# Kernel tuning notes

Measured on AMD Instinct MI355X. Metric: run time of the kernel, lower is better.

Reference implementation:

```python
import jax, jax.numpy as jnp
import numpy as np

N_USERS = 50000
N_ITEMS = 50000
E = 400000
S = 128   # in_feats_s (memory / GRU hidden)
T = 64    # in_feats_t (time encoding dim)
ED = 64   # edge feature dim
M = 2 * S + T + ED  # in_feats_m = 384

_BASIS_FREQ = jnp.asarray(1.0 / 10 ** np.linspace(0, 9, T), dtype=jnp.float32)


def time_encode(ts):
    # cos(ts * freq + phase), phase == 0
    return jnp.cos(ts[:, None] * _BASIS_FREQ[None, :])


def mean_message(src_mem, dst_mem, ts, e, src, dst, n_dst):
    # mail per edge: [E, 2S + T + ED]
    mail = jnp.concatenate(
        [src_mem[src], dst_mem[dst], time_encode(ts), e], axis=1)
    s = jax.ops.segment_sum(mail, dst, num_segments=n_dst)
    cnt = jax.ops.segment_sum(jnp.ones_like(ts), dst, num_segments=n_dst)
    return s / jnp.maximum(cnt, 1.0)[:, None]


def gru_step(x, h, w_ih, w_hh, b_ih, b_hh):
    # single-step PyTorch GRU; gate order r, z, n
    gi = x @ w_ih.T + b_ih
    gh = h @ w_hh.T + b_hh
    ir, iz, i_n = jnp.split(gi, 3, axis=1)
    hr, hz, h_n = jnp.split(gh, 3, axis=1)
    r = jax.nn.sigmoid(ir + hr)
    z = jax.nn.sigmoid(iz + hz)
    n = jnp.tanh(i_n + r * h_n)
    return (1.0 - z) * n + z * h


def setup_inputs() -> dict:
    key = jax.random.key(0)
    ks = jax.random.split(key, 16)
    sc = 1.0 / np.sqrt(S)
    return {
        "si":   jax.random.normal(ks[0], (N_USERS, S), jnp.float32),
        "sj":   jax.random.normal(ks[1], (N_ITEMS, S), jnp.float32),
        "si_r": jax.random.normal(ks[2], (N_ITEMS, S), jnp.float32),
        "sj_r": jax.random.normal(ks[3], (N_USERS, S), jnp.float32),
        "t":    jax.random.uniform(ks[4], (E,), jnp.float32),
        "t_r":  jax.random.uniform(ks[5], (E,), jnp.float32),
        "e":    jax.random.normal(ks[6], (E, ED), jnp.float32),
        "e_r":  jax.random.normal(ks[7], (E, ED), jnp.float32),
        "w_ih": jax.random.normal(ks[8], (3 * S, M), jnp.float32) * sc,
        "w_hh": jax.random.normal(ks[9], (3 * S, S), jnp.float32) * sc,
        "b_ih": jax.random.normal(ks[10], (3 * S,), jnp.float32) * sc,
        "b_hh": jax.random.normal(ks[11], (3 * S,), jnp.float32) * sc,
        "src_g":  jax.random.randint(ks[12], (E,), 0, N_USERS, jnp.int32),
        "dst_g":  jax.random.randint(ks[13], (E,), 0, N_ITEMS, jnp.int32),
        "src_gr": jax.random.randint(ks[14], (E,), 0, N_ITEMS, jnp.int32),
        "dst_gr": jax.random.randint(ks[15], (E,), 0, N_USERS, jnp.int32),
    }


def reference(si, sj, si_r, sj_r, t, t_r, e, e_r,
              w_ih, w_hh, b_ih, b_hh,
              src_g, dst_g, src_gr, dst_gr):
    # g: user -> item; g_r: item -> user
    mj = mean_message(si, sj, t, e, src_g, dst_g, N_ITEMS)       # messages to items
    mi = mean_message(si_r, sj_r, t_r, e_r, src_gr, dst_gr, N_USERS)  # messages to users
    si_out = gru_step(mi, sj_r, w_ih, w_hh, b_ih, b_hh)  # user memory update
    sj_out = gru_step(mj, sj, w_ih, w_hh, b_ih, b_hh)    # item memory update
    return (si_out, sj_out)
```

## Files before the change

### kernel.cpp

```cpp
#include <hip/hip_runtime.h>
#include <math.h>

#define NUSERS 50000
#define NITEMS 50000
#define NTOT   100000
#define NNODE  50000
#define NCHUNK 196
#define MTILES 6250
#define KDIM   512

typedef __attribute__((ext_vector_type(4))) float f32x4;
typedef __attribute__((ext_vector_type(8))) short short8;
typedef unsigned int u32;

#define AS1 __attribute__((address_space(1)))
#define AS3 __attribute__((address_space(3)))

static __device__ __forceinline__ unsigned short f2bf(float f) {
  unsigned int u = __float_as_uint(f);
  u += 0x7fffu + ((u >> 16) & 1u);
  return (unsigned short)(u >> 16);
}

static __device__ __forceinline__ void gload_lds16(const void* g, void* l) {
  __builtin_amdgcn_global_load_lds((const AS1 u32*)g, (AS3 u32*)l, 16, 0, 0);
}

__global__ void pack_w_kernel(const float* __restrict__ w_ih,
                              const float* __restrict__ w_hh,
                              const float* __restrict__ b_ih,
                              const float* __restrict__ b_hh,
                              unsigned short* __restrict__ Wb,
                              float* __restrict__ bb) {
  int idx = blockIdx.x * 256 + threadIdx.x;
  int j = idx & 7, l = (idx >> 3) & 63, ktt = idx >> 9;
  int kt = ktt & 15, tt = ktt >> 4;
  int g = tt * 16 + (l & 15);
  int k = kt * 32 + (l >> 4) * 8 + j;
  float v;
  if (g < 256)      v = (k < 384) ? w_ih[g * 384 + k] : w_hh[g * 128 + (k - 384)];
  else if (g < 384) v = (k < 384) ? w_ih[g * 384 + k] : 0.0f;
  else              v = (k < 384) ? 0.0f : w_hh[(g - 128) * 128 + (k - 384)];
  Wb[idx] = f2bf(v);
  if (idx < 512) {
    float b = (idx < 256) ? (b_ih[idx] + b_hh[idx])
            : (idx < 384) ? b_ih[idx]
                          : b_hh[idx - 128];
    bb[idx] = b;
  }
}

__global__ void hist_kernel(const int* __restrict__ dst_g,
                            const int* __restrict__ dst_gr,
                            int* __restrict__ deg_j, int* __restrict__ deg_i, int E) {
  int i = blockIdx.x * 256 + threadIdx.x;
  if (i < E) atomicAdd(&deg_j[dst_g[i]], 1);
  else if (i < 2 * E) atomicAdd(&deg_i[dst_gr[i - E]], 1);
}

__global__ void chunksum_kernel(const int* __restrict__ deg_j,
                                const int* __restrict__ deg_i,
                                int* __restrict__ csum) {
  int c = blockIdx.x;
  const int* deg = (c < NCHUNK) ? deg_j : deg_i;
  int cc = (c < NCHUNK) ? c : c - NCHUNK;
  int t = threadIdx.x;
  int idx = cc * 256 + t;
  int v = (idx < NNODE) ? deg[idx] : 0;
  for (int off = 32; off; off >>= 1) v += __shfl_down(v, off, 64);
  __shared__ int wsum[4];
  if ((t & 63) == 0) wsum[t >> 6] = v;
  __syncthreads();
  if (t == 0) csum[c] = wsum[0] + wsum[1] + wsum[2] + wsum[3];
}

__global__ void chunkscan_kernel(const int* __restrict__ csum, int* __restrict__ coff) {
  int d = blockIdx.x;
  const int* cs = csum + d * NCHUNK;
  int* co = coff + d * NCHUNK;
  int t = threadIdx.x, lane = t & 63, w = t >> 6;
  int v = (t < NCHUNK) ? cs[t] : 0;
  int x = v;
  for (int off = 1; off < 64; off <<= 1) {
    int y = __shfl_up(x, off, 64);
    if (lane >= off) x += y;
  }
  __shared__ int wt[4];
  if (lane == 63) wt[w] = x;
  __syncthreads();
  int add = 0;
  for (int k = 0; k < 4; ++k) if (k < w) add += wt[k];
  if (t < NCHUNK) co[t] = add + x - v;
}

__global__ void localscan_kernel(const int* __restrict__ deg_j,
                                 const int* __restrict__ deg_i,
                                 const int* __restrict__ coff,
                                 int* __restrict__ rs_j, int* __restrict__ cur_j,
                                 int* __restrict__ rs_i, int* __restrict__ cur_i) {
  int c = blockIdx.x;
  bool dj = c < NCHUNK;
  const int* deg = dj ? deg_j : deg_i;
  int cc = dj ? c : c - NCHUNK;
  int* rs = dj ? rs_j : rs_i;
  int* cur = dj ? cur_j : cur_i;
  int base = coff[c];
  int t = threadIdx.x, lane = t & 63, w = t >> 6;
  int idx = cc * 256 + t;
  int v = (idx < NNODE) ? deg[idx] : 0;
  int x = v;
  for (int off = 1; off < 64; off <<= 1) {
    int y = __shfl_up(x, off, 64);
    if (lane >= off) x += y;
  }
  __shared__ int wt[4];
  if (lane == 63) wt[w] = x;
  __syncthreads();
  int add = 0;
  for (int k = 0; k < 4; ++k) if (k < w) add += wt[k];
  int ex = base + add + x - v;
  if (idx < NNODE) { rs[idx] = ex; cur[idx] = ex; }
}

__global__ void fill_kernel(const int* __restrict__ src_g, const int* __restrict__ dst_g,
                            const float* __restrict__ t,
                            const int* __restrict__ src_gr, const int* __restrict__ dst_gr,
                            const float* __restrict__ t_r,
                            int* __restrict__ cur_j, int* __restrict__ cur_i,
                            int4* __restrict__ recP_j, int4* __restrict__ recP_i,
                            int E) {
  int i = blockIdx.x * 256 + threadIdx.x;
  if (i < E) {
    int pos = atomicAdd(&cur_j[dst_g[i]], 1);
    recP_j[pos] = make_int4(src_g[i], i, __float_as_int(t[i]), 0);
  } else if (i < 2 * E) {
    int k = i - E;
    int pos = atomicAdd(&cur_i[dst_gr[k]], 1);
    recP_i[pos] = make_int4(src_gr[k], k, __float_as_int(t_r[k]), 0);
  }
}

__global__ __launch_bounds__(256) void gather_kernel(
    const float* __restrict__ si, const float* __restrict__ sj,
    const float* __restrict__ si_r, const float* __restrict__ sj_r,
    const float* __restrict__ e, const float* __restrict__ e_r,
    const int* __restrict__ rs_j, const int* __restrict__ rs_i,
    const int* __restrict__ deg_j, const int* __restrict__ deg_i,
    const int4* __restrict__ recP_j, const int4* __restrict__ recP_i,
    unsigned short* __restrict__ Xb) {
  __shared__ __align__(16) unsigned short rowbuf[4][512];
  int wid = threadIdx.x >> 6, lane = threadIdx.x & 63;
  int node = blockIdx.x * 4 + wid;
  bool user = node < NUSERS;
  int idx = user ? node : node - NUSERS;
  const float* smem = user ? si_r : si;
  const float* h    = user ? sj_r : sj;
  const float* ef   = user ? e_r : e;
  int start = __builtin_amdgcn_readfirstlane((user ? rs_i : rs_j)[idx]);
  int deg   = __builtin_amdgcn_readfirstlane((user ? deg_i : deg_j)[idx]);
  const int4* rec = user ? recP_i : recP_j;

  float freq = __expf((float)lane * -0.3289407276f);
  float a0 = 0.f, a1 = 0.f, a2 = 0.f, a3 = 0.f;

  for (int i = 0; i < deg; i += 4) {
    int i1 = (i + 1 < deg) ? i + 1 : deg - 1;
    int i2 = (i + 2 < deg) ? i + 2 : deg - 1;
    int i3 = (i + 3 < deg) ? i + 3 : deg - 1;
    int4 r0 = rec[start + i];
    int4 r1 = rec[start + i1];
    int4 r2 = rec[start + i2];
    int4 r3 = rec[start + i3];
    float w1 = (i + 1 < deg) ? 1.0f : 0.0f;
    float w2 = (i + 2 < deg) ? 1.0f : 0.0f;
    float w3 = (i + 3 < deg) ? 1.0f : 0.0f;

    float x00 = smem[(size_t)r0.x * 128 + lane];
    float x01 = smem[(size_t)r0.x * 128 + 64 + lane];
    float f0  = ef[(size_t)r0.y * 64 + lane];
    float x10 = smem[(size_t)r1.x * 128 + lane];
    float x11 = smem[(size_t)r1.x * 128 + 64 + lane];
    float f1  = ef[(size_t)r1.y * 64 + lane];
    float x20 = smem[(size_t)r2.x * 128 + lane];
    float x21 = smem[(size_t)r2.x * 128 + 64 + lane];
    float f2  = ef[(size_t)r2.y * 64 + lane];
    float x30 = smem[(size_t)r3.x * 128 + lane];
    float x31 = smem[(size_t)r3.x * 128 + 64 + lane];
    float f3  = ef[(size_t)r3.y * 64 + lane];

    float c0 = __cosf(__int_as_float(r0.z) * freq);
    float c1 = __cosf(__int_as_float(r1.z) * freq);
    float c2 = __cosf(__int_as_float(r2.z) * freq);
    float c3 = __cosf(__int_as_float(r3.z) * freq);

    a0 += x00 + w1 * x10 + w2 * x20 + w3 * x30;
    a1 += x01 + w1 * x11 + w2 * x21 + w3 * x31;
    a2 += c0  + w1 * c1  + w2 * c2  + w3 * c3;
    a3 += f0  + w1 * f1  + w2 * f2  + w3 * f3;
  }

  float invc = (deg > 0) ? 1.0f / (float)deg : 0.0f;
  float hz   = (deg > 0) ? 1.0f : 0.0f;
  float h0 = h[(size_t)idx * 128 + lane];
  float h1 = h[(size_t)idx * 128 + 64 + lane];

  unsigned short* rb = rowbuf[wid];
  rb[lane]        = f2bf(a0 * invc);
  rb[64  + lane]  = f2bf(a1 * invc);
  rb[128 + lane]  = f2bf(h0 * hz);
  rb[192 + lane]  = f2bf(h1 * hz);
  rb[256 + lane]  = f2bf(a2 * invc);
  rb[320 + lane]  = f2bf(a3 * invc);
  rb[384 + lane]  = f2bf(h0);
  rb[448 + lane]  = f2bf(h1);
  __syncthreads();

  int rt = node >> 4, m = node & 15;
  int kt = lane >> 2, q = lane & 3;
  short8 vv = *(const short8*)(rb + lane * 8);
  *(short8*)(Xb + (((size_t)rt * 16 + kt) * 64 + q * 16 + m) * 8) = vv;
}

__global__ __launch_bounds__(512, 2) void gemm_gru_kernel(
    const unsigned short* __restrict__ Xb,
    const unsigned short* __restrict__ Wb,
    const float* __restrict__ bb,
    const float* __restrict__ sj_r,
    const float* __restrict__ sj,
    float* __restrict__ out) {
  __shared__ __align__(16) unsigned short sB[32768];
  int wid = threadIdx.x >> 6, lane = threadIdx.x & 63;
  int mtile = blockIdx.x * 8 + wid;
  bool valid = mtile < MTILES;
  int col16 = lane & 15, quad = lane >> 4;

  f32x4 acc[32];
#pragma unroll
  for (int t = 0; t < 32; ++t) acc[t] = (f32x4)0.0f;

  const unsigned short* Abase = Xb + (size_t)(valid ? mtile : 0) * 8192;

  for (int s = 0; s < 8; ++s) {
#pragma unroll
    for (int i = 0; i < 8; ++i) {
      int c = wid * 8 + i;
      int tt = c >> 1, kt = s * 2 + (c & 1);
      const unsigned short* g = Wb + ((size_t)(tt * 16 + kt) * 64 + lane) * 8;
      gload_lds16(g, sB + c * 512);
    }
    __syncthreads();
    if (valid) {
      short8 a0 = *(const short8*)(Abase + (size_t)(s * 2) * 512 + lane * 8);
      short8 a1 = *(const short8*)(Abase + (size_t)(s * 2 + 1) * 512 + lane * 8);
#pragma unroll
      for (int t = 0; t < 32; ++t) {
        short8 b0 = *(const short8*)(sB + (t * 2) * 512 + lane * 8);
        short8 b1 = *(const short8*)(sB + (t * 2 + 1) * 512 + lane * 8);
        acc[t] = __builtin_amdgcn_mfma_f32_16x16x32_bf16(a0, b0, acc[t], 0, 0, 0);
        acc[t] = __builtin_amdgcn_mfma_f32_16x16x32_bf16(a1, b1, acc[t], 0, 0, 0);
      }
    }
    __syncthreads();
  }

  if (!valid) return;
  int m0 = mtile * 16;
#pragma unroll
  for (int t = 0; t < 8; ++t) {
    int c = t * 16 + col16;
    float bbr = bb[c], bbz = bb[128 + c], bbn = bb[256 + c], bbh = bb[384 + c];
#pragma unroll
    for (int r = 0; r < 4; ++r) {
      int row = m0 + quad * 4 + r;
      float rp  = acc[t][r]      + bbr;
      float zp  = acc[t + 8][r]  + bbz;
      float inp = acc[t + 16][r] + bbn;
      float hnp = acc[t + 24][r] + bbh;
      float rg = 1.0f / (1.0f + __expf(-rp));
      float zg = 1.0f / (1.0f + __expf(-zp));
      float ng = tanhf(inp + rg * hnp);
      float hv = (row < NUSERS) ? sj_r[(size_t)row * 128 + c]
                                : sj[(size_t)(row - NUSERS) * 128 + c];
      out[(size_t)row * 128 + c] = (1.0f - zg) * ng + zg * hv;
    }
  }
}

extern "C" void kernel_launch(void* const* d_in, const int* in_sizes, int n_in,
                              void* d_out, int out_size, void* d_ws, size_t ws_size,
                              hipStream_t stream) {
  const float* si   = (const float*)d_in[0];
  const float* sj   = (const float*)d_in[1];
  const float* si_r = (const float*)d_in[2];
  const float* sj_r = (const float*)d_in[3];
  const float* t    = (const float*)d_in[4];
  const float* t_r  = (const float*)d_in[5];
  const float* e    = (const float*)d_in[6];
  const float* e_r  = (const float*)d_in[7];
  const float* w_ih = (const float*)d_in[8];
  const float* w_hh = (const float*)d_in[9];
  const float* b_ih = (const float*)d_in[10];
  const float* b_hh = (const float*)d_in[11];
  const int* src_g  = (const int*)d_in[12];
  const int* dst_g  = (const int*)d_in[13];
  const int* src_gr = (const int*)d_in[14];
  const int* dst_gr = (const int*)d_in[15];
  int E = in_sizes[4];

  unsigned short* Xb = (unsigned short*)d_ws;
  unsigned short* Wb = Xb + (size_t)MTILES * 8192;
  float* bb   = (float*)(Wb + 262144);
  int* deg_j  = (int*)(bb + 512);
  int* deg_i  = deg_j + NNODE;
  int* rs_j   = deg_i + NNODE;
  int* rs_i   = rs_j + NNODE;
  int* cur_j  = rs_i + NNODE;
  int* cur_i  = cur_j + NNODE;
  int* csum   = cur_i + NNODE;
  int* coff   = csum + 2 * NCHUNK;
  int4* recP_j = (int4*)(coff + 2 * NCHUNK);
  int4* recP_i = recP_j + E;

  hipMemsetAsync(deg_j, 0, 2 * NNODE * sizeof(int), stream);

  pack_w_kernel<<<(512 * 512) / 256, 256, 0, stream>>>(w_ih, w_hh, b_ih, b_hh, Wb, bb);

  int blks2E = (2 * E + 255) / 256;
  hist_kernel<<<blks2E, 256, 0, stream>>>(dst_g, dst_gr, deg_j, deg_i, E);
  chunksum_kernel<<<2 * NCHUNK, 256, 0, stream>>>(deg_j, deg_i, csum);
  chunkscan_kernel<<<2, 256, 0, stream>>>(csum, coff);
  localscan_kernel<<<2 * NCHUNK, 256, 0, stream>>>(deg_j, deg_i, coff, rs_j, cur_j, rs_i, cur_i);
  fill_kernel<<<blks2E, 256, 0, stream>>>(src_g, dst_g, t, src_gr, dst_gr, t_r,
                                          cur_j, cur_i, recP_j, recP_i, E);

  gather_kernel<<<NTOT / 4, 256, 0, stream>>>(si, sj, si_r, sj_r, e, e_r,
                                              rs_j, rs_i, deg_j, deg_i,
                                              recP_j, recP_i, Xb);

  float* out = (float*)d_out;
  gemm_gru_kernel<<<(MTILES + 7) / 8, 512, 0, stream>>>(Xb, Wb, bb, sj_r, sj, out);
}
```

Before: 660.6 us.

## Pre-cast source memories to bf16 and batch edge records via readlane in gather

Adds a kernel that converts si and si_r to bf16 once, so the gather kernel reads half the bytes per gathered source row. The gather loop now loads up to 64 edge records in one coalesced wave load and broadcasts them with readlane, unrolling 8 edges at a time. The h row is read as float2 and LDS writes are packed in pairs. The __syncthreads is removed, which is safe only because each wave reads back its own rowbuf slot. Costs are an extra full pass over si/si_r, more workspace, and bf16 rounding of source memories before averaging.

```diff
diff --git a/kernel.cpp b/kernel.cpp
--- a/kernel.cpp
+++ b/kernel.cpp
@@ -20,6 +20,10 @@
   unsigned int u = __float_as_uint(f);
   u += 0x7fffu + ((u >> 16) & 1u);
   return (unsigned short)(u >> 16);
+}
+
+static __device__ __forceinline__ u32 pack2(float x, float y) {
+  return (u32)f2bf(x) | ((u32)f2bf(y) << 16);
 }
 
 static __device__ __forceinline__ void gload_lds16(const void* g, void* l) {
@@ -50,6 +54,22 @@
   }
 }
 
+__global__ void cast_mem_kernel(const float* __restrict__ si,
+                                const float* __restrict__ si_r,
+                                unsigned short* __restrict__ si_b,
+                                unsigned short* __restrict__ sir_b) {
+  int i = blockIdx.x * 256 + threadIdx.x;
+  const float* src; unsigned short* dst; int off;
+  if (i < 800000) { src = si;   dst = si_b;  off = i; }
+  else            { src = si_r; dst = sir_b; off = i - 800000; }
+  const f32x4* p = (const f32x4*)(src + (size_t)off * 8);
+  f32x4 a = p[0], b = p[1];
+  short8 o;
+  o[0] = f2bf(a[0]); o[1] = f2bf(a[1]); o[2] = f2bf(a[2]); o[3] = f2bf(a[3]);
+  o[4] = f2bf(b[0]); o[5] = f2bf(b[1]); o[6] = f2bf(b[2]); o[7] = f2bf(b[3]);
+  *(short8*)(dst + (size_t)off * 8) = o;
+}
+
 __global__ void hist_kernel(const int* __restrict__ dst_g,
                             const int* __restrict__ dst_gr,
                             int* __restrict__ deg_j, int* __restrict__ deg_i, int E) {
@@ -141,8 +161,8 @@
 }
 
 __global__ __launch_bounds__(256) void gather_kernel(
-    const float* __restrict__ si, const float* __restrict__ sj,
-    const float* __restrict__ si_r, const float* __restrict__ sj_r,
+    const unsigned short* __restrict__ si_b, const unsigned short* __restrict__ sir_b,
+    const float* __restrict__ sj, const float* __restrict__ sj_r,
     const float* __restrict__ e, const float* __restrict__ e_r,
     const int* __restrict__ rs_j, const int* __restrict__ rs_i,
     const int* __restrict__ deg_j, const int* __restrict__ deg_i,
@@ -153,7 +173,7 @@
   int node = blockIdx.x * 4 + wid;
   bool user = node < NUSERS;
   int idx = user ? node : node - NUSERS;
-  const float* smem = user ? si_r : si;
+  const unsigned short* smem = user ? sir_b : si_b;
   const float* h    = user ? sj_r : sj;
   const float* ef   = user ? e_r : e;
   int start = __builtin_amdgcn_readfirstlane((user ? rs_i : rs_j)[idx]);
@@ -161,64 +181,98 @@
   const int4* rec = user ? recP_i : recP_j;
 
   float freq = __expf((float)lane * -0.3289407276f);
-  float a0 = 0.f, a1 = 0.f, a2 = 0.f, a3 = 0.f;
-
-  for (int i = 0; i < deg; i += 4) {
-    int i1 = (i + 1 < deg) ? i + 1 : deg - 1;
-    int i2 = (i + 2 < deg) ? i + 2 : deg - 1;
-    int i3 = (i + 3 < deg) ? i + 3 : deg - 1;
-    int4 r0 = rec[start + i];
-    int4 r1 = rec[start + i1];
-    int4 r2 = rec[start + i2];
-    int4 r3 = rec[start + i3];
-    float w1 = (i + 1 < deg) ? 1.0f : 0.0f;
-    float w2 = (i + 2 < deg) ? 1.0f : 0.0f;
-    float w3 = (i + 3 < deg) ? 1.0f : 0.0f;
-
-    float x00 = smem[(size_t)r0.x * 128 + lane];
-    float x01 = smem[(size_t)r0.x * 128 + 64 + lane];
-    float f0  = ef[(size_t)r0.y * 64 + lane];
-    float x10 = smem[(size_t)r1.x * 128 + lane];
-    float x11 = smem[(size_t)r1.x * 128 + 64 + lane];
-    float f1  = ef[(size_t)r1.y * 64 + lane];
-    float x20 = smem[(size_t)r2.x * 128 + lane];
-    float x21 = smem[(size_t)r2.x * 128 + 64 + lane];
-    float f2  = ef[(size_t)r2.y * 64 + lane];
-    float x30 = smem[(size_t)r3.x * 128 + lane];
-    float x31 = smem[(size_t)r3.x * 128 + 64 + lane];
-    float f3  = ef[(size_t)r3.y * 64 + lane];
-
-    float c0 = __cosf(__int_as_float(r0.z) * freq);
-    float c1 = __cosf(__int_as_float(r1.z) * freq);
-    float c2 = __cosf(__int_as_float(r2.z) * freq);
-    float c3 = __cosf(__int_as_float(r3.z) * freq);
-
-    a0 += x00 + w1 * x10 + w2 * x20 + w3 * x30;
-    a1 += x01 + w1 * x11 + w2 * x21 + w3 * x31;
-    a2 += c0  + w1 * c1  + w2 * c2  + w3 * c3;
-    a3 += f0  + w1 * f1  + w2 * f2  + w3 * f3;
+  float2 hvf = *(const float2*)(h + (size_t)idx * 128 + 2 * lane);
+
+  float asx = 0.f, asy = 0.f;
+  float at  = 0.f;
+  float ae  = 0.f;
+
+  for (int base = 0; base < deg; base += 64) {
+    int nn = deg - base; if (nn > 64) nn = 64;
+    int cl = (lane < nn) ? base + lane : base + nn - 1;
+    int4 r = rec[start + cl];
+    for (int j0 = 0; j0 < nn; j0 += 8) {
+      int j1 = (j0 + 1 < nn) ? j0 + 1 : nn - 1;
+      int j2 = (j0 + 2 < nn) ? j0 + 2 : nn - 1;
+      int j3 = (j0 + 3 < nn) ? j0 + 3 : nn - 1;
+      int j4 = (j0 + 4 < nn) ? j0 + 4 : nn - 1;
+      int j5 = (j0 + 5 < nn) ? j0 + 5 : nn - 1;
+      int j6 = (j0 + 6 < nn) ? j0 + 6 : nn - 1;
+      int j7 = (j0 + 7 < nn) ? j0 + 7 : nn - 1;
+      float w1 = (j0 + 1 < nn) ? 1.0f : 0.0f;
+      float w2 = (j0 + 2 < nn) ? 1.0f : 0.0f;
+      float w3 = (j0 + 3 < nn) ? 1.0f : 0.0f;
+      float w4 = (j0 + 4 < nn) ? 1.0f : 0.0f;
+      float w5 = (j0 + 5 < nn) ? 1.0f : 0.0f;
+      float w6 = (j0 + 6 < nn) ? 1.0f : 0.0f;
+      float w7 = (j0 + 7 < nn) ? 1.0f : 0.0f;
+
+      int s0 = __builtin_amdgcn_readlane(r.x, j0), e0 = __builtin_amdgcn_readlane(r.y, j0);
+      int s1 = __builtin_amdgcn_readlane(r.x, j1), e1 = __builtin_amdgcn_readlane(r.y, j1);
+      int s2 = __builtin_amdgcn_readlane(r.x, j2), e2 = __builtin_amdgcn_readlane(r.y, j2);
+      int s3 = __builtin_amdgcn_readlane(r.x, j3), e3 = __builtin_amdgcn_readlane(r.y, j3);
+      int s4 = __builtin_amdgcn_readlane(r.x, j4), e4 = __builtin_amdgcn_readlane(r.y, j4);
+      int s5 = __builtin_amdgcn_readlane(r.x, j5), e5 = __builtin_amdgcn_readlane(r.y, j5);
+      int s6 = __builtin_amdgcn_readlane(r.x, j6), e6 = __builtin_amdgcn_readlane(r.y, j6);
+      int s7 = __builtin_amdgcn_readlane(r.x, j7), e7 = __builtin_amdgcn_readlane(r.y, j7);
+
+      u32 v0 = *(const u32*)(smem + ((size_t)s0 << 7) + 2 * lane);
+      u32 v1 = *(const u32*)(smem + ((size_t)s1 << 7) + 2 * lane);
+      u32 v2 = *(const u32*)(smem + ((size_t)s2 << 7) + 2 * lane);
+      u32 v3 = *(const u32*)(smem + ((size_t)s3 << 7) + 2 * lane);
+      u32 v4 = *(const u32*)(smem + ((size_t)s4 << 7) + 2 * lane);
+      u32 v5 = *(const u32*)(smem + ((size_t)s5 << 7) + 2 * lane);
+      u32 v6 = *(const u32*)(smem + ((size_t)s6 << 7) + 2 * lane);
+      u32 v7 = *(const u32*)(smem + ((size_t)s7 << 7) + 2 * lane);
+      float f0 = ef[((size_t)e0 << 6) + lane];
+      float f1 = ef[((size_t)e1 << 6) + lane];
+      float f2 = ef[((size_t)e2 << 6) + lane];
+      float f3 = ef[((size_t)e3 << 6) + lane];
+      float f4 = ef[((size_t)e4 << 6) + lane];
+      float f5 = ef[((size_t)e5 << 6) + lane];
+      float f6 = ef[((size_t)e6 << 6) + lane];
+      float f7 = ef[((size_t)e7 << 6) + lane];
+
+      float c0 = __cosf(__int_as_float(__builtin_amdgcn_readlane(r.z, j0)) * freq);
+      float c1 = __cosf(__int_as_float(__builtin_amdgcn_readlane(r.z, j1)) * freq);
+      float c2 = __cosf(__int_as_float(__builtin_amdgcn_readlane(r.z, j2)) * freq);
+      float c3 = __cosf(__int_as_float(__builtin_amdgcn_readlane(r.z, j3)) * freq);
+      float c4 = __cosf(__int_as_float(__builtin_amdgcn_readlane(r.z, j4)) * freq);
+      float c5 = __cosf(__int_as_float(__builtin_amdgcn_readlane(r.z, j5)) * freq);
+      float c6 = __cosf(__int_as_float(__builtin_amdgcn_readlane(r.z, j6)) * freq);
+      float c7 = __cosf(__int_as_float(__builtin_amdgcn_readlane(r.z, j7)) * freq);
+
+      float l0 = __uint_as_float(v0 << 16), g0 = __uint_as_float(v0 & 0xffff0000u);
+      float l1 = __uint_as_float(v1 << 16), g1 = __uint_as_float(v1 & 0xffff0000u);
+      float l2 = __uint_as_float(v2 << 16), g2 = __uint_as_float(v2 & 0xffff0000u);
+      float l3 = __uint_as_float(v3 << 16), g3 = __uint_as_float(v3 & 0xffff0000u);
+      float l4 = __uint_as_float(v4 << 16), g4 = __uint_as_float(v4 & 0xffff0000u);
+      float l5 = __uint_as_float(v5 << 16), g5 = __uint_as_float(v5 & 0xffff0000u);
+      float l6 = __uint_as_float(v6 << 16), g6 = __uint_as_float(v6 & 0xffff0000u);
+      float l7 = __uint_as_float(v7 << 16), g7 = __uint_as_float(v7 & 0xffff0000u);
+
+      asx += l0 + w1 * l1 + w2 * l2 + w3 * l3 + w4 * l4 + w5 * l5 + w6 * l6 + w7 * l7;
+      asy += g0 + w1 * g1 + w2 * g2 + w3 * g3 + w4 * g4 + w5 * g5 + w6 * g6 + w7 * g7;
+      at  += c0 + w1 * c1 + w2 * c2 + w3 * c3 + w4 * c4 + w5 * c5 + w6 * c6 + w7 * c7;
+      ae  += f0 + w1 * f1 + w2 * f2 + w3 * f3 + w4 * f4 + w5 * f5 + w6 * f6 + w7 * f7;
+    }
   }
 
   float invc = (deg > 0) ? 1.0f / (float)deg : 0.0f;
   float hz   = (deg > 0) ? 1.0f : 0.0f;
-  float h0 = h[(size_t)idx * 128 + lane];
-  float h1 = h[(size_t)idx * 128 + 64 + lane];
 
   unsigned short* rb = rowbuf[wid];
-  rb[lane]        = f2bf(a0 * invc);
-  rb[64  + lane]  = f2bf(a1 * invc);
-  rb[128 + lane]  = f2bf(h0 * hz);
-  rb[192 + lane]  = f2bf(h1 * hz);
-  rb[256 + lane]  = f2bf(a2 * invc);
-  rb[320 + lane]  = f2bf(a3 * invc);
-  rb[384 + lane]  = f2bf(h0);
-  rb[448 + lane]  = f2bf(h1);
-  __syncthreads();
+  u32* rb32 = (u32*)rb;
+  rb32[lane]       = pack2(asx * invc, asy * invc);
+  rb32[64 + lane]  = pack2(hvf.x * hz, hvf.y * hz);
+  rb[256 + lane]   = f2bf(at * invc);
+  rb[320 + lane]   = f2bf(ae * invc);
+  rb32[192 + lane] = pack2(hvf.x, hvf.y);
 
   int rt = node >> 4, m = node & 15;
-  int kt = lane >> 2, q = lane & 3;
+  int kt2 = lane >> 2, q2 = lane & 3;
   short8 vv = *(const short8*)(rb + lane * 8);
-  *(short8*)(Xb + (((size_t)rt * 16 + kt) * 64 + q * 16 + m) * 8) = vv;
+  *(short8*)(Xb + (((size_t)rt * 16 + kt2) * 64 + q2 * 16 + m) * 8) = vv;
 }
 
 __global__ __launch_bounds__(512, 2) void gemm_gru_kernel(
@@ -320,10 +374,13 @@
   int* coff   = csum + 2 * NCHUNK;
   int4* recP_j = (int4*)(coff + 2 * NCHUNK);
   int4* recP_i = recP_j + E;
+  unsigned short* si_b  = (unsigned short*)(recP_i + E);
+  unsigned short* sir_b = si_b + 6400000;
 
   hipMemsetAsync(deg_j, 0, 2 * NNODE * sizeof(int), stream);
 
   pack_w_kernel<<<(512 * 512) / 256, 256, 0, stream>>>(w_ih, w_hh, b_ih, b_hh, Wb, bb);
+  cast_mem_kernel<<<6250, 256, 0, stream>>>(si, si_r, si_b, sir_b);
 
   int blks2E = (2 * E + 255) / 256;
   hist_kernel<<<blks2E, 256, 0, stream>>>(dst_g, dst_gr, deg_j, deg_i, E);
@@ -333,7 +390,7 @@
   fill_kernel<<<blks2E, 256, 0, stream>>>(src_g, dst_g, t, src_gr, dst_gr, t_r,
                                           cur_j, cur_i, recP_j, recP_i, E);
 
-  gather_kernel<<<NTOT / 4, 256, 0, stream>>>(si, sj, si_r, sj_r, e, e_r,
+  gather_kernel<<<NTOT / 4, 256, 0, stream>>>(si_b, sir_b, sj, sj_r, e, e_r,
                                               rs_j, rs_i, deg_j, deg_i,
                                               recP_j, recP_i, Xb);
 
```

Result: faster. 647.6 us (-2.0%).
